# Performance work log

Hardware: AMD Instinct MI355X
Metric: run time of the kernel (lower is better)

The kernel has to match this reference:

```python
import jax, jax.numpy as jnp
import numpy as np
import math

IN_F = 4096
OUT_F = 4096
NUM_FREQ = 16
RANK = 2
N_TOK = 8192


def setup_inputs() -> dict:
    key = jax.random.key(0)
    ks = jax.random.split(key, 10)
    x = jax.random.normal(ks[0], (N_TOK, IN_F), dtype=jnp.float32)
    amp = jax.random.normal(ks[1], (NUM_FREQ,), dtype=jnp.float32) * 0.1
    rf = jax.random.normal(ks[2], (NUM_FREQ,), dtype=jnp.float32) * 2.0
    cf = jax.random.normal(ks[3], (NUM_FREQ,), dtype=jnp.float32) * 2.0
    rp = jax.random.normal(ks[4], (NUM_FREQ,), dtype=jnp.float32) * 0.5
    cp = jax.random.normal(ks[5], (NUM_FREQ,), dtype=jnp.float32) * 0.5
    lora_A = jax.random.normal(ks[6], (OUT_F, RANK), dtype=jnp.float32) * 0.01
    lora_B = jax.random.normal(ks[7], (RANK, IN_F), dtype=jnp.float32) * 0.01
    alpha = jnp.float32(0.5)
    beta = jnp.float32(0.5)
    bias = jnp.zeros((OUT_F,), dtype=jnp.float32)
    return {"x": x, "amp": amp, "rf": rf, "cf": cf, "rp": rp, "cp": cp,
            "lora_A": lora_A, "lora_B": lora_B, "alpha": alpha, "beta": beta,
            "bias": bias}


def reference(x, amp, rf, cf, rp, cp, lora_A, lora_B, alpha, beta, bias):
    out_f, in_f = lora_A.shape[0], lora_B.shape[1]
    two_pi = 2.0 * math.pi
    r = jnp.linspace(0.0, two_pi, out_f, dtype=jnp.float32)  # [out_f]
    c = jnp.linspace(0.0, two_pi, in_f, dtype=jnp.float32)   # [in_f]
    # Fourier weight synthesis: sum_k amp[k] * outer(sin(r*rf[k]+rp[k]), cos(c*cf[k]+cp[k]))
    S = jnp.sin(r[None, :] * rf[:, None] + rp[:, None])  # [nf, out_f]
    C = jnp.cos(c[None, :] * cf[:, None] + cp[:, None])  # [nf, in_f]
    W_fourier = jnp.einsum('k,ko,ki->oi', amp, S, C)     # [out_f, in_f]
    W_lora = lora_A @ lora_B                              # [out_f, in_f]
    std = math.sqrt(2.0 / (in_f + out_f))
    a = jax.nn.sigmoid(alpha)
    b = jax.nn.sigmoid(beta)
    W = a * jnp.tanh(W_fourier) * std + b * jnp.tanh(W_lora) * std
    return x @ W.T + bias
```

## Files before the change

### kernel.cpp

```cpp
#include <hip/hip_runtime.h>
#include <hip/hip_bf16.h>
#include <cstdint>

typedef __attribute__((ext_vector_type(4))) float f32x4;
typedef __attribute__((ext_vector_type(4))) int i32x4;

#define IN_F 4096
#define OUT_F 4096
#define N_TOK 8192
#define NUM_FREQ 16
#define RROWS 4


__device__ inline float fast_tanh(float x) {
    float ax = fabsf(x);
    float e = __expf(2.0f * ax);
    float t = 1.0f - 2.0f / (e + 1.0f);
    return copysignf(t, x);
}

__device__ inline void load_lds16(const void* g, void* l) {
    __builtin_amdgcn_global_load_lds(
        (const __attribute__((address_space(1))) void*)(uintptr_t)g,
        (__attribute__((address_space(3))) void*)(uint32_t)(uintptr_t)l,
        16, 0, 0);
}

__device__ inline int q8(float v, float s) {
    int q = (int)rintf(v * s);
    return min(127, max(-127, q));
}

__device__ inline unsigned int pack4(int q0, int q1, int q2, int q3) {
    return (q0 & 255) | ((q1 & 255) << 8) | ((q2 & 255) << 16) |
           ((q3 & 255) << 24);
}

__global__ __launch_bounds__(256)
void prep(const float* __restrict__ x, signed char* __restrict__ xq,
          float* __restrict__ sx, const float* __restrict__ amp,
          const float* __restrict__ rf, const float* __restrict__ cf,
          const float* __restrict__ rp, const float* __restrict__ cp,
          const float* __restrict__ lA, const float* __restrict__ lB,
          const float* __restrict__ alpha, const float* __restrict__ beta,
          signed char* __restrict__ wq, float* __restrict__ sw) {
    const int tid = threadIdx.x;
    const int wave = tid >> 6;
    const int lane = tid & 63;
    __shared__ float s_s[RROWS][NUM_FREQ];
    __shared__ float red[RROWS][4];

    if (blockIdx.x < OUT_F / RROWS) {
        const int o0 = blockIdx.x * RROWS;
        const float step = 6.28318530717958647692f / 4095.0f;
        if (tid < RROWS * NUM_FREQ) {
            const int r = tid >> 4;
            const int k = tid & 15;
            s_s[r][k] =
                amp[k] * __sinf(step * (float)(o0 + r) * rf[k] + rp[k]);
        }
        __syncthreads();

        const int g = lane >> 2;
        const int q = lane & 3;

        float cfr[4], cpr[4];
#pragma unroll
        for (int e = 0; e < 4; ++e) {
            cfr[e] = cf[q * 4 + e];
            cpr[e] = cp[q * 4 + e];
        }
        float skr[RROWS][4];
#pragma unroll
        for (int r = 0; r < RROWS; ++r)
#pragma unroll
            for (int e = 0; e < 4; ++e) skr[r][e] = s_s[r][q * 4 + e];

        const float sa = 1.0f / (1.0f + __expf(-alpha[0]));
        const float sb = 1.0f / (1.0f + __expf(-beta[0]));
        const float stdv = 0.015625f;
        float a0r[RROWS], a1r[RROWS];
#pragma unroll
        for (int r = 0; r < RROWS; ++r) {
            a0r[r] = lA[(o0 + r) * 2 + 0];
            a1r[r] = lA[(o0 + r) * 2 + 1];
        }

        const int ibw = wave * 1024;
        float w[RROWS][16];

#pragma unroll
        for (int j = 0; j < 16; ++j) {
#pragma unroll
            for (int sq = 0; sq < 4; ++sq) {
                const int i = ibw + (j * 4 + sq) * 16 + g;
                const float ci = step * (float)i;
                float cv[4];
#pragma unroll
                for (int e = 0; e < 4; ++e)
                    cv[e] = __cosf(ci * cfr[e] + cpr[e]);
#pragma unroll
                for (int r = 0; r < RROWS; ++r) {
                    float p = skr[r][0] * cv[0] + skr[r][1] * cv[1] +
                              skr[r][2] * cv[2] + skr[r][3] * cv[3];
                    p += __shfl_xor(p, 1);
                    p += __shfl_xor(p, 2);
                    if (q == sq) w[r][j] = p;
                }
            }
        }

#pragma unroll
        for (int j = 0; j < 16; ++j) {
            const int i = ibw + (j * 4 + q) * 16 + g;
            const float b0 = lB[i];
            const float b1 = lB[IN_F + i];
#pragma unroll
            for (int r = 0; r < RROWS; ++r) {
                const float wl = a0r[r] * b0 + a1r[r] * b1;
                w[r][j] = sa * stdv * fast_tanh(w[r][j]) +
                          sb * stdv * fast_tanh(wl);
            }
        }

        float m[RROWS];
#pragma unroll
        for (int r = 0; r < RROWS; ++r) {
            float mm = 0.0f;
#pragma unroll
            for (int j = 0; j < 16; ++j) mm = fmaxf(mm, fabsf(w[r][j]));
#pragma unroll
            for (int off = 32; off > 0; off >>= 1)
                mm = fmaxf(mm, __shfl_xor(mm, off));
            m[r] = mm;
        }
        if (lane == 0) {
#pragma unroll
            for (int r = 0; r < RROWS; ++r) red[r][wave] = m[r];
        }
        __syncthreads();
#pragma unroll
        for (int r = 0; r < RROWS; ++r) {
            float mm = fmaxf(fmaxf(red[r][0], red[r][1]),
                             fmaxf(red[r][2], red[r][3]));
            m[r] = fmaxf(mm, 1e-20f);
        }

#pragma unroll
        for (int r = 0; r < RROWS; ++r) {
            const float s = 127.0f / m[r];
            signed char* wrow = wq + (size_t)(o0 + r) * IN_F;
#pragma unroll
            for (int j = 0; j < 16; ++j) {
                const int i = ibw + (j * 4 + q) * 16 + g;
                wrow[i] = (signed char)q8(w[r][j], s);
            }
        }
        if (tid == 0) {
#pragma unroll
            for (int r = 0; r < RROWS; ++r) sw[o0 + r] = m[r] / 127.0f;
        }
    } else {
        const int t = blockIdx.x - OUT_F / RROWS;
        const f32x4* xr = (const f32x4*)(x + (size_t)t * IN_F);
        f32x4 v[4];
#pragma unroll
        for (int j = 0; j < 4; ++j) v[j] = xr[tid + 256 * j];
        float m = 0.0f;
#pragma unroll
        for (int j = 0; j < 4; ++j)
#pragma unroll
            for (int e = 0; e < 4; ++e) m = fmaxf(m, fabsf(v[j][e]));
#pragma unroll
        for (int off = 32; off > 0; off >>= 1)
            m = fmaxf(m, __shfl_xor(m, off));
        if (lane == 0) red[0][wave] = m;
        __syncthreads();
        m = fmaxf(fmaxf(red[0][0], red[0][1]), fmaxf(red[0][2], red[0][3]));
        m = fmaxf(m, 1e-20f);
        const float s = 127.0f / m;
        unsigned int* orow = (unsigned int*)(xq + (size_t)t * IN_F);
#pragma unroll
        for (int j = 0; j < 4; ++j)
            orow[tid + 256 * j] =
                pack4(q8(v[j][0], s), q8(v[j][1], s), q8(v[j][2], s),
                      q8(v[j][3], s));
        if (tid == 0) sx[t] = m / 127.0f;
    }
}

#define BM 256
#define BN 128
#define BKB 128
#define SUBK 64

__global__ __launch_bounds__(256, 2)
void gemm_i8(const signed char* __restrict__ A, const signed char* __restrict__ B,
             const float* __restrict__ sx, const float* __restrict__ sw,
             const float* __restrict__ bias, float* __restrict__ C,
             int M, int N, int K) {
    __shared__ signed char sA[2][BM * SUBK];
    __shared__ signed char sB[2][BN * SUBK];

    const int tid = threadIdx.x;
    const int wave = tid >> 6;
    const int lane = tid & 63;

    const int bm = blockIdx.y * BM;
    const int bn = blockIdx.x * BN;

    const int srow = lane >> 2;
    const int scol = (((lane & 3) ^ ((lane >> 3) & 3)) << 4);

    const signed char* gA = A + (size_t)(bm + wave * 16 + srow) * K + scol;
    const signed char* gB = B + (size_t)(bn + wave * 16 + srow) * K + scol;

    const int lm = lane & 15;
    const int quad = lane >> 4;
    const int kq = ((quad ^ ((lm >> 1) & 3)) << 4);

    const int wm = (wave & 1) * 128;
    const int wn = (wave >> 1) * 64;
    const int aoff = (wm + lm) * SUBK + kq;
    const int boff = (wn + lm) * SUBK + kq;

    i32x4 acc[8][4] = {};

    for (int k0 = 0; k0 < K; k0 += BKB) {
#pragma unroll
        for (int h = 0; h < 2; ++h) {
            const int kk = k0 + h * SUBK;
#pragma unroll
            for (int c = 0; c < 4; ++c)
                load_lds16(gA + (size_t)c * 64 * K + kk,
                           &sA[h][(wave * 16 + c * 64) * SUBK]);
#pragma unroll
            for (int c = 0; c < 2; ++c)
                load_lds16(gB + (size_t)c * 64 * K + kk,
                           &sB[h][(wave * 16 + c * 64) * SUBK]);
        }
        __syncthreads();

#pragma unroll
        for (int h = 0; h < 2; ++h) {
            i32x4 af[8], bv[4];
#pragma unroll
            for (int i = 0; i < 8; ++i)
                af[i] = *(const i32x4*)&sA[h][aoff + i * 16 * SUBK];
#pragma unroll
            for (int i = 0; i < 4; ++i)
                bv[i] = *(const i32x4*)&sB[h][boff + i * 16 * SUBK];

#pragma unroll
            for (int im = 0; im < 8; ++im)
#pragma unroll
                for (int in = 0; in < 4; ++in)
                    acc[im][in] = __builtin_amdgcn_mfma_i32_16x16x64_i8(
                        af[im], bv[in], acc[im][in], 0, 0, 0);
        }

        __syncthreads();
    }

    float sxv[8][4];
#pragma unroll
    for (int im = 0; im < 8; ++im)
#pragma unroll
        for (int r = 0; r < 4; ++r)
            sxv[im][r] = sx[bm + wm + im * 16 + quad * 4 + r];

#pragma unroll
    for (int in = 0; in < 4; ++in) {
        const int cn = bn + wn + in * 16 + lm;
        const float bv_ = bias[cn];
        const float scw = sw[cn];
#pragma unroll
        for (int im = 0; im < 8; ++im) {
            const int rm = bm + wm + im * 16 + quad * 4;
#pragma unroll
            for (int r = 0; r < 4; ++r)
                C[(size_t)(rm + r) * N + cn] =
                    (float)acc[im][in][r] * (sxv[im][r] * scw) + bv_;
        }
    }
}

extern "C" void kernel_launch(void* const* d_in, const int* in_sizes, int n_in,
                              void* d_out, int out_size, void* d_ws,
                              size_t ws_size, hipStream_t stream) {
    const float* x = (const float*)d_in[0];
    const float* amp = (const float*)d_in[1];
    const float* rf = (const float*)d_in[2];
    const float* cf = (const float*)d_in[3];
    const float* rp = (const float*)d_in[4];
    const float* cp = (const float*)d_in[5];
    const float* lA = (const float*)d_in[6];
    const float* lB = (const float*)d_in[7];
    const float* alpha = (const float*)d_in[8];
    const float* beta = (const float*)d_in[9];
    const float* bias = (const float*)d_in[10];
    float* out = (float*)d_out;

    signed char* wq = (signed char*)d_ws;
    signed char* xq = wq + (size_t)OUT_F * IN_F;
    float* sw = (float*)(xq + (size_t)N_TOK * IN_F);
    float* sx = sw + OUT_F;

    prep<<<OUT_F / RROWS + N_TOK, 256, 0, stream>>>(
        x, xq, sx, amp, rf, cf, rp, cp, lA, lB, alpha, beta, wq, sw);
    gemm_i8<<<dim3(OUT_F / BN, N_TOK / BM), 256, 0, stream>>>(
        xq, wq, sx, sw, bias, out, N_TOK, OUT_F, IN_F);
}
```

Measured before the change: 430.0 us.

## Enlarge int8 GEMM tile to 256x256 with 4-slot async LDS pipeline

Doubles the N tile to 256 and runs 512 threads (8 waves) per block. Each 64-wide K sub-step gets its own LDS slot in a 128KB buffer, and global loads are issued two K-steps ahead. Explicit vmcnt/lgkmcnt waits, raw barriers and sched_barriers replace the old load-then-sync loop, and MFMA priority is raised. The aim is to overlap global-to-LDS traffic with MFMA work and raise data reuse per block. The cost is the large LDS footprint, which limits occupancy to one block per CU, and fragile hand-tuned wait counts.

```diff
diff --git a/kernel.cpp b/kernel.cpp
--- a/kernel.cpp
+++ b/kernel.cpp
@@ -190,17 +190,16 @@
 }
 
 #define BM 256
-#define BN 128
+#define BN 256
 #define BKB 128
 #define SUBK 64
 
-__global__ __launch_bounds__(256, 2)
+__global__ __launch_bounds__(512, 2)
 void gemm_i8(const signed char* __restrict__ A, const signed char* __restrict__ B,
              const float* __restrict__ sx, const float* __restrict__ sw,
              const float* __restrict__ bias, float* __restrict__ C,
              int M, int N, int K) {
-    __shared__ signed char sA[2][BM * SUBK];
-    __shared__ signed char sB[2][BN * SUBK];
+    __shared__ signed char lds[131072];
 
     const int tid = threadIdx.x;
     const int wave = tid >> 6;
@@ -214,6 +213,7 @@
 
     const signed char* gA = A + (size_t)(bm + wave * 16 + srow) * K + scol;
     const signed char* gB = B + (size_t)(bn + wave * 16 + srow) * K + scol;
+    const size_t rowK = (size_t)128 * K;
 
     const int lm = lane & 15;
     const int quad = lane >> 4;
@@ -224,42 +224,70 @@
     const int aoff = (wm + lm) * SUBK + kq;
     const int boff = (wn + lm) * SUBK + kq;
 
+    const int NT = K >> 7;
+
+    auto STAGE = [&](int slot, int kk) {
+        signed char* la = &lds[(slot << 14) + wave * 1024];
+        signed char* lb = &lds[65536 + (slot << 14) + wave * 1024];
+        load_lds16(gA + kk, la);
+        load_lds16(gA + rowK + kk, la + 8192);
+        load_lds16(gB + kk, lb);
+        load_lds16(gB + rowK + kk, lb + 8192);
+    };
+
     i32x4 acc[8][4] = {};
 
-    for (int k0 = 0; k0 < K; k0 += BKB) {
+    STAGE(0, 0);
+    STAGE(1, SUBK);
+    STAGE(2, BKB);
+    STAGE(3, BKB + SUBK);
+
+    for (int t = 0; t < NT; ++t) {
 #pragma unroll
         for (int h = 0; h < 2; ++h) {
-            const int kk = k0 + h * SUBK;
-#pragma unroll
-            for (int c = 0; c < 4; ++c)
-                load_lds16(gA + (size_t)c * 64 * K + kk,
-                           &sA[h][(wave * 16 + c * 64) * SUBK]);
-#pragma unroll
-            for (int c = 0; c < 2; ++c)
-                load_lds16(gB + (size_t)c * 64 * K + kk,
-                           &sB[h][(wave * 16 + c * 64) * SUBK]);
-        }
-        __syncthreads();
-
-#pragma unroll
-        for (int h = 0; h < 2; ++h) {
+            const int slot = ((t & 1) << 1) | h;
+            if (h == 0) {
+                if (t < NT - 1)
+                    asm volatile("s_waitcnt vmcnt(12)" ::: "memory");
+                else
+                    asm volatile("s_waitcnt vmcnt(4)" ::: "memory");
+            } else {
+                if (t < NT - 2)
+                    asm volatile("s_waitcnt vmcnt(12)" ::: "memory");
+                else if (t == NT - 2)
+                    asm volatile("s_waitcnt vmcnt(8)" ::: "memory");
+                else
+                    asm volatile("s_waitcnt vmcnt(0)" ::: "memory");
+            }
+            __builtin_amdgcn_s_barrier();
+            __builtin_amdgcn_sched_barrier(0);
+
+            const signed char* pa = &lds[(slot << 14)];
+            const signed char* pb = &lds[65536 + (slot << 14)];
             i32x4 af[8], bv[4];
 #pragma unroll
             for (int i = 0; i < 8; ++i)
-                af[i] = *(const i32x4*)&sA[h][aoff + i * 16 * SUBK];
+                af[i] = *(const i32x4*)(pa + aoff + i * 1024);
 #pragma unroll
             for (int i = 0; i < 4; ++i)
-                bv[i] = *(const i32x4*)&sB[h][boff + i * 16 * SUBK];
-
+                bv[i] = *(const i32x4*)(pb + boff + i * 1024);
+            asm volatile("s_waitcnt lgkmcnt(0)" ::: "memory");
+            __builtin_amdgcn_sched_barrier(0);
+            __builtin_amdgcn_s_barrier();
+            __builtin_amdgcn_sched_barrier(0);
+
+            if (t + 2 < NT) STAGE(slot, (t + 2) * BKB + h * SUBK);
+            __builtin_amdgcn_sched_barrier(0);
+
+            __builtin_amdgcn_s_setprio(1);
 #pragma unroll
             for (int im = 0; im < 8; ++im)
 #pragma unroll
                 for (int in = 0; in < 4; ++in)
                     acc[im][in] = __builtin_amdgcn_mfma_i32_16x16x64_i8(
                         af[im], bv[in], acc[im][in], 0, 0, 0);
-        }
-
-        __syncthreads();
+            __builtin_amdgcn_s_setprio(0);
+        }
     }
 
     float sxv[8][4];
@@ -308,6 +336,6 @@
 
     prep<<<OUT_F / RROWS + N_TOK, 256, 0, stream>>>(
         x, xq, sx, amp, rf, cf, rp, cp, lA, lB, alpha, beta, wq, sw);
-    gemm_i8<<<dim3(OUT_F / BN, N_TOK / BM), 256, 0, stream>>>(
+    gemm_i8<<<dim3(OUT_F / BN, N_TOK / BM), 512, 0, stream>>>(
         xq, wq, sx, sw, bias, out, N_TOK, OUT_F, IN_F);
 }
```

After: 426.8 us. About the same (-0.8%).

## Restructure int8 GEMM into 256x256 tiles with 4-stage LDS pipeline

Applied to the files above, without the earlier changes.

The int8 GEMM moves to 256x256 output tiles with 512 threads (8 waves) and a 4-slot, 128KB LDS ring. Global-to-LDS loads are issued three k-slices ahead, using explicit vmcnt waits and split barriers, so memory traffic overlaps MFMA work. Each slice is split into two halves with s_setprio around the MFMA bursts to interleave loads and compute. This is meant to raise arithmetic intensity and hide load latency, at the cost of heavy LDS use (128KB, likely one block per CU despite launch_bounds asking for 2) and fragile hand-counted waitcnt logic.

```diff
diff --git a/kernel.cpp b/kernel.cpp
--- a/kernel.cpp
+++ b/kernel.cpp
@@ -190,17 +190,15 @@
 }
 
 #define BM 256
-#define BN 128
-#define BKB 128
+#define BN 256
 #define SUBK 64
 
-__global__ __launch_bounds__(256, 2)
+__global__ __launch_bounds__(512, 2)
 void gemm_i8(const signed char* __restrict__ A, const signed char* __restrict__ B,
              const float* __restrict__ sx, const float* __restrict__ sw,
              const float* __restrict__ bias, float* __restrict__ C,
              int M, int N, int K) {
-    __shared__ signed char sA[2][BM * SUBK];
-    __shared__ signed char sB[2][BN * SUBK];
+    __shared__ signed char lds[131072];
 
     const int tid = threadIdx.x;
     const int wave = tid >> 6;
@@ -214,6 +212,7 @@
 
     const signed char* gA = A + (size_t)(bm + wave * 16 + srow) * K + scol;
     const signed char* gB = B + (size_t)(bn + wave * 16 + srow) * K + scol;
+    const size_t rowK = (size_t)128 * K;
 
     const int lm = lane & 15;
     const int quad = lane >> 4;
@@ -224,43 +223,75 @@
     const int aoff = (wm + lm) * SUBK + kq;
     const int boff = (wn + lm) * SUBK + kq;
 
+    const int NT = K >> 6;
+
+    auto STAGE_H0 = [&](int slot, int tt) {
+        load_lds16(gA + (size_t)tt * SUBK, &lds[(slot << 14) + wave * 1024]);
+        load_lds16(gB + (size_t)tt * SUBK,
+                   &lds[65536 + (slot << 14) + wave * 1024]);
+    };
+    auto STAGE_H1 = [&](int slot, int tt) {
+        load_lds16(gA + rowK + (size_t)tt * SUBK,
+                   &lds[(slot << 14) + wave * 1024 + 8192]);
+        load_lds16(gB + rowK + (size_t)tt * SUBK,
+                   &lds[65536 + (slot << 14) + wave * 1024 + 8192]);
+    };
+
     i32x4 acc[8][4] = {};
-
-    for (int k0 = 0; k0 < K; k0 += BKB) {
-#pragma unroll
-        for (int h = 0; h < 2; ++h) {
-            const int kk = k0 + h * SUBK;
-#pragma unroll
-            for (int c = 0; c < 4; ++c)
-                load_lds16(gA + (size_t)c * 64 * K + kk,
-                           &sA[h][(wave * 16 + c * 64) * SUBK]);
-#pragma unroll
-            for (int c = 0; c < 2; ++c)
-                load_lds16(gB + (size_t)c * 64 * K + kk,
-                           &sB[h][(wave * 16 + c * 64) * SUBK]);
-        }
-        __syncthreads();
-
-#pragma unroll
-        for (int h = 0; h < 2; ++h) {
-            i32x4 af[8], bv[4];
-#pragma unroll
-            for (int i = 0; i < 8; ++i)
-                af[i] = *(const i32x4*)&sA[h][aoff + i * 16 * SUBK];
-#pragma unroll
-            for (int i = 0; i < 4; ++i)
-                bv[i] = *(const i32x4*)&sB[h][boff + i * 16 * SUBK];
-
-#pragma unroll
-            for (int im = 0; im < 8; ++im)
-#pragma unroll
-                for (int in = 0; in < 4; ++in)
-                    acc[im][in] = __builtin_amdgcn_mfma_i32_16x16x64_i8(
-                        af[im], bv[in], acc[im][in], 0, 0, 0);
-        }
-
-        __syncthreads();
+    i32x4 afl[4], afh[4], bva[4], bvb[4];
+
+#define SLICE(T, BVN)                                                       \
+    {                                                                       \
+        const int slot_ = (T) & 3;                                          \
+        const signed char* pa_ = &lds[slot_ << 14];                         \
+        const signed char* pb_ = &lds[65536 + (slot_ << 14)];               \
+        _Pragma("unroll") for (int i = 0; i < 4; ++i)                       \
+            afl[i] = *(const i32x4*)(pa_ + aoff + i * 1024);                \
+        _Pragma("unroll") for (int i = 0; i < 4; ++i)                       \
+            BVN[i] = *(const i32x4*)(pb_ + boff + i * 1024);                \
+        if ((T) + 3 < NT) STAGE_H0(((T) + 3) & 3, (T) + 3);                 \
+        __builtin_amdgcn_s_barrier();                                       \
+        asm volatile("s_waitcnt lgkmcnt(0)" ::: "memory");                  \
+        __builtin_amdgcn_sched_barrier(0);                                  \
+        __builtin_amdgcn_s_setprio(1);                                      \
+        _Pragma("unroll") for (int im = 0; im < 4; ++im)                    \
+            _Pragma("unroll") for (int in = 0; in < 4; ++in)                \
+                acc[im][in] = __builtin_amdgcn_mfma_i32_16x16x64_i8(        \
+                    afl[im], BVN[in], acc[im][in], 0, 0, 0);                \
+        __builtin_amdgcn_s_setprio(0);                                      \
+        __builtin_amdgcn_s_barrier();                                       \
+        _Pragma("unroll") for (int i = 0; i < 4; ++i)                       \
+            afh[i] = *(const i32x4*)(pa_ + aoff + 4096 + i * 1024);         \
+        if ((T) + 3 < NT) STAGE_H1(((T) + 3) & 3, (T) + 3);                 \
+        if ((T) < NT - 3)                                                   \
+            asm volatile("s_waitcnt vmcnt(8)" ::: "memory");                \
+        else if ((T) == NT - 3)                                             \
+            asm volatile("s_waitcnt vmcnt(4)" ::: "memory");                \
+        else                                                                \
+            asm volatile("s_waitcnt vmcnt(0)" ::: "memory");                \
+        __builtin_amdgcn_s_barrier();                                       \
+        asm volatile("s_waitcnt lgkmcnt(0)" ::: "memory");                  \
+        __builtin_amdgcn_sched_barrier(0);                                  \
+        __builtin_amdgcn_s_setprio(1);                                      \
+        _Pragma("unroll") for (int im = 0; im < 4; ++im)                    \
+            _Pragma("unroll") for (int in = 0; in < 4; ++in)                \
+                acc[im + 4][in] = __builtin_amdgcn_mfma_i32_16x16x64_i8(    \
+                    afh[im], BVN[in], acc[im + 4][in], 0, 0, 0);            \
+        __builtin_amdgcn_s_setprio(0);                                      \
+        __builtin_amdgcn_s_barrier();                                       \
     }
+
+    STAGE_H0(0, 0); STAGE_H1(0, 0);
+    STAGE_H0(1, 1); STAGE_H1(1, 1);
+    STAGE_H0(2, 2); STAGE_H1(2, 2);
+    asm volatile("s_waitcnt vmcnt(8)" ::: "memory");
+    __builtin_amdgcn_s_barrier();
+
+    for (int t = 0; t < NT; t += 2) {
+        SLICE(t, bva);
+        SLICE(t + 1, bvb);
+    }
+#undef SLICE
 
     float sxv[8][4];
 #pragma unroll
@@ -308,6 +339,6 @@
 
     prep<<<OUT_F / RROWS + N_TOK, 256, 0, stream>>>(
         x, xq, sx, amp, rf, cf, rp, cp, lA, lB, alpha, beta, wq, sw);
-    gemm_i8<<<dim3(OUT_F / BN, N_TOK / BM), 256, 0, stream>>>(
+    gemm_i8<<<dim3(OUT_F / BN, N_TOK / BM), 512, 0, stream>>>(
         xq, wq, sx, sw, bias, out, N_TOK, OUT_F, IN_F);
 }
```

After: 428.0 us. Within noise of the previous version (-0.5%).

## Switch int8 GEMM to 32x32x32 MFMA and swizzle block order for L2 reuse

Applied to the files above, without the earlier changes.

Replaces the 16x16x64 int8 MFMA tiling with 32x32x32 MFMA tiles, restructuring the LDS fragment loads, the accumulator layout and the epilogue row mapping to match. Larger MFMA tiles cut the number of LDS reads per FLOP. The block index is also remapped so groups of consecutive blocks share A/B tiles, aiming at better L2 locality. The new fragment and output indexing must line up exactly with the 32x32 MFMA layout, and the hardcoded grid constants (32 columns of blocks, groups of 8) assume the fixed problem size.

```diff
diff --git a/kernel.cpp b/kernel.cpp
--- a/kernel.cpp
+++ b/kernel.cpp
@@ -4,6 +4,7 @@
 
 typedef __attribute__((ext_vector_type(4))) float f32x4;
 typedef __attribute__((ext_vector_type(4))) int i32x4;
+typedef __attribute__((ext_vector_type(16))) int i32x16;
 
 #define IN_F 4096
 #define OUT_F 4096
@@ -206,25 +207,33 @@
     const int wave = tid >> 6;
     const int lane = tid & 63;
 
-    const int bm = blockIdx.y * BM;
-    const int bn = blockIdx.x * BN;
+    const int id = blockIdx.y * 32 + blockIdx.x;
+    const int sid = (id & 7) * 128 + (id >> 3);
+    const int bm = (sid >> 5) * BM;
+    const int bn = (sid & 31) * BN;
 
     const int srow = lane >> 2;
     const int scol = (((lane & 3) ^ ((lane >> 3) & 3)) << 4);
 
     const signed char* gA = A + (size_t)(bm + wave * 16 + srow) * K + scol;
     const signed char* gB = B + (size_t)(bn + wave * 16 + srow) * K + scol;
-
-    const int lm = lane & 15;
-    const int quad = lane >> 4;
-    const int kq = ((quad ^ ((lm >> 1) & 3)) << 4);
+    const size_t rowK = (size_t)64 * K;
+
+    const int r32 = lane & 31;
+    const int l5 = lane >> 5;
+    const int swz = (lane >> 1) & 3;
 
     const int wm = (wave & 1) * 128;
     const int wn = (wave >> 1) * 64;
-    const int aoff = (wm + lm) * SUBK + kq;
-    const int boff = (wn + lm) * SUBK + kq;
-
-    i32x4 acc[8][4] = {};
+
+    int au[2][2], bu[2][2];
+#pragma unroll
+    for (int ks = 0; ks < 2; ++ks) {
+        au[ks][0] = ((((ks << 1) | l5) ^ swz) << 4);
+        bu[ks][0] = au[ks][0];
+    }
+
+    i32x16 acc[4][2] = {};
 
     for (int k0 = 0; k0 < K; k0 += BKB) {
 #pragma unroll
@@ -232,55 +241,73 @@
             const int kk = k0 + h * SUBK;
 #pragma unroll
             for (int c = 0; c < 4; ++c)
-                load_lds16(gA + (size_t)c * 64 * K + kk,
+                load_lds16(gA + (size_t)c * rowK + kk,
                            &sA[h][(wave * 16 + c * 64) * SUBK]);
 #pragma unroll
             for (int c = 0; c < 2; ++c)
-                load_lds16(gB + (size_t)c * 64 * K + kk,
+                load_lds16(gB + (size_t)c * rowK + kk,
                            &sB[h][(wave * 16 + c * 64) * SUBK]);
         }
         __syncthreads();
 
 #pragma unroll
         for (int h = 0; h < 2; ++h) {
-            i32x4 af[8], bv[4];
-#pragma unroll
-            for (int i = 0; i < 8; ++i)
-                af[i] = *(const i32x4*)&sA[h][aoff + i * 16 * SUBK];
-#pragma unroll
-            for (int i = 0; i < 4; ++i)
-                bv[i] = *(const i32x4*)&sB[h][boff + i * 16 * SUBK];
-
-#pragma unroll
-            for (int im = 0; im < 8; ++im)
-#pragma unroll
-                for (int in = 0; in < 4; ++in)
-                    acc[im][in] = __builtin_amdgcn_mfma_i32_16x16x64_i8(
-                        af[im], bv[in], acc[im][in], 0, 0, 0);
+            i32x4 af[4][2], bv[2][2];
+#pragma unroll
+            for (int mt = 0; mt < 4; ++mt)
+#pragma unroll
+                for (int ks = 0; ks < 2; ++ks)
+                    af[mt][ks] = *(const i32x4*)&sA[h][(wm + mt * 32 + r32) *
+                                                           SUBK +
+                                                       au[ks][0]];
+#pragma unroll
+            for (int nt = 0; nt < 2; ++nt)
+#pragma unroll
+                for (int ks = 0; ks < 2; ++ks)
+                    bv[nt][ks] = *(const i32x4*)&sB[h][(wn + nt * 32 + r32) *
+                                                           SUBK +
+                                                       bu[ks][0]];
+
+#pragma unroll
+            for (int mt = 0; mt < 4; ++mt)
+#pragma unroll
+                for (int nt = 0; nt < 2; ++nt)
+#pragma unroll
+                    for (int ks = 0; ks < 2; ++ks)
+                        acc[mt][nt] = __builtin_amdgcn_mfma_i32_32x32x32_i8(
+                            af[mt][ks], bv[nt][ks], acc[mt][nt], 0, 0, 0);
         }
 
         __syncthreads();
     }
 
-    float sxv[8][4];
-#pragma unroll
-    for (int im = 0; im < 8; ++im)
-#pragma unroll
-        for (int r = 0; r < 4; ++r)
-            sxv[im][r] = sx[bm + wm + im * 16 + quad * 4 + r];
-
-#pragma unroll
-    for (int in = 0; in < 4; ++in) {
-        const int cn = bn + wn + in * 16 + lm;
-        const float bv_ = bias[cn];
+    float sxr[4][16];
+#pragma unroll
+    for (int mt = 0; mt < 4; ++mt)
+#pragma unroll
+        for (int c = 0; c < 4; ++c)
+#pragma unroll
+            for (int e = 0; e < 4; ++e)
+                sxr[mt][c * 4 + e] =
+                    sx[bm + wm + mt * 32 + 8 * c + 4 * l5 + e];
+
+#pragma unroll
+    for (int nt = 0; nt < 2; ++nt) {
+        const int cn = bn + wn + nt * 32 + r32;
+        const float bb = bias[cn];
         const float scw = sw[cn];
 #pragma unroll
-        for (int im = 0; im < 8; ++im) {
-            const int rm = bm + wm + im * 16 + quad * 4;
-#pragma unroll
-            for (int r = 0; r < 4; ++r)
-                C[(size_t)(rm + r) * N + cn] =
-                    (float)acc[im][in][r] * (sxv[im][r] * scw) + bv_;
+        for (int mt = 0; mt < 4; ++mt) {
+#pragma unroll
+            for (int c = 0; c < 4; ++c)
+#pragma unroll
+                for (int e = 0; e < 4; ++e) {
+                    const int row = bm + wm + mt * 32 + 8 * c + 4 * l5 + e;
+                    C[(size_t)row * N + cn] =
+                        (float)acc[mt][nt][c * 4 + e] *
+                            (sxr[mt][c * 4 + e] * scw) +
+                        bb;
+                }
         }
     }
 }
```

Measured after the change: 418.4 us. 1.03x faster.
